# Optimization experiments

Measured on AMD Instinct MI355X. Metric: run time of the kernel, lower is better.

## Reference

```python
import jax, jax.numpy as jnp
import numpy as np

NEG_RATIO = 3.0
EPS = 1e-4
WEIGHT = 1.0
LOG_CLAMP = -100.0  # torch.nn.BCELoss clamps log terms at -100

B, H, W = 32, 768, 768


def setup_inputs() -> dict:
    key = jax.random.key(0)
    k1, k2 = jax.random.split(key)
    gt_centerness = jax.random.uniform(k1, (B, H, W), dtype=jnp.float32)
    pred_binary = jax.random.uniform(k2, (B, 1, H, W), dtype=jnp.float32)
    return {"gt_centerness": gt_centerness, "pred_binary": pred_binary}


def reference(gt_centerness, pred_binary):
    b = pred_binary.shape[0]
    # squeeze pred channel dim, flatten per-batch then logically treat as flat
    pred = pred_binary.reshape(b, -1)          # [B, N]
    gt = gt_centerness.reshape(b, -1)          # [B, N]
    dtype = pred.dtype

    pos_mask = gt >= 0.9                        # hard positives
    ignore_mask = (gt >= 0.8) & (gt < 0.9)      # ignore band
    mask = 1.0 - ignore_mask.astype(dtype)      # keep = 1, ignore = 0

    # elementwise BCE with torch-style log clamping
    loss = -(gt * jnp.clip(jnp.log(pred), LOG_CLAMP, None)
             + (1.0 - gt) * jnp.clip(jnp.log(1.0 - pred), LOG_CLAMP, None))

    pos = jnp.sum(pos_mask)                                  # scalar int
    ignore = jnp.sum(ignore_mask)
    total = gt.size
    neg = total - pos - ignore

    positive_sum = jnp.sum(loss * mask * pos_mask.astype(dtype))

    neg_mask = (1.0 - pos_mask.astype(dtype)) * mask
    neg_loss = (loss * neg_mask).reshape(-1)                 # [B*N]

    # k = min(max(pos,1) * neg_ratio, neg), as an integer
    k = jnp.minimum(jnp.maximum(pos, 1).astype(dtype) * NEG_RATIO,
                    neg.astype(dtype))
    k = jnp.floor(k).astype(jnp.int32)

    # top-k sum via descending sort + rank mask (k is traced -> fixed-shape)
    sorted_neg = jnp.sort(neg_loss)[::-1]
    ranks = jnp.arange(sorted_neg.shape[0], dtype=jnp.int32)
    topk_sum = jnp.sum(jnp.where(ranks < k, sorted_neg, jnp.zeros((), dtype)))

    denom = pos.astype(dtype) + k.astype(dtype) + EPS
    return WEIGHT * (NEG_RATIO * positive_sum + topk_sum) / denom
```

## Files before the change

kernel.cpp:

```cpp
#include <hip/hip_runtime.h>

#define NBINS    2048
#define REPL     4
#define THREADS  256
#define BLOCKS   512
#define CNTSH    44

__device__ __forceinline__ void process_elem(
    float g, float p,
    unsigned int& posc, float& ps,
    unsigned long long* hist, unsigned int repl)
{
    float nlp = fminf(-__logf(p), 100.0f);
    float nlq = fminf(-__logf(1.0f - p), 100.0f);
    float loss = fmaf(g, nlp - nlq, nlq);

    bool isPos = (g >= 0.9f);
    bool isNeg = (g < 0.8f);
    posc += isPos;
    if (isPos) ps += loss;
    if (isNeg) {
        unsigned int b = 0;
        if (loss > 0.0f) {
            b = __float_as_uint(loss) >> 20;
            if (b > NBINS - 1) b = NBINS - 1;
        }
        unsigned long long q =
            (unsigned long long)(unsigned int)(fmaf(loss, 1048576.0f, 0.5f));
        atomicAdd(&hist[(b << 2) | repl], (1ull << CNTSH) | q);
    }
}

__device__ __forceinline__ void process4(
    float4 g, float4 p,
    unsigned int& posc, float& ps,
    unsigned long long* hist, unsigned int repl)
{
    process_elem(g.x, p.x, posc, ps, hist, repl);
    process_elem(g.y, p.y, posc, ps, hist, repl);
    process_elem(g.z, p.z, posc, ps, hist, repl);
    process_elem(g.w, p.w, posc, ps, hist, repl);
}

__global__ __launch_bounds__(THREADS) void pass1(
    const float* __restrict__ gt, const float* __restrict__ pred,
    unsigned int* __restrict__ counts, unsigned long long* __restrict__ sums,
    unsigned int* __restrict__ posCnt, double* __restrict__ psum,
    int n4, int nTail, long long tailBase)
{
    __shared__ unsigned long long hist[NBINS * REPL];
    for (int i = threadIdx.x; i < NBINS * REPL; i += THREADS) hist[i] = 0ull;
    __syncthreads();

    unsigned int posc = 0;
    float ps = 0.0f;
    const unsigned int repl = threadIdx.x & (REPL - 1);

    const float4* g4p = (const float4*)gt;
    const float4* p4p = (const float4*)pred;
    const int stride = gridDim.x * blockDim.x;
    int i = blockIdx.x * blockDim.x + threadIdx.x;

    for (; i + 3 * stride < n4; i += 4 * stride) {
        float4 g0 = g4p[i];              float4 p0 = p4p[i];
        float4 g1 = g4p[i + stride];     float4 p1 = p4p[i + stride];
        float4 g2 = g4p[i + 2 * stride]; float4 p2 = p4p[i + 2 * stride];
        float4 g3 = g4p[i + 3 * stride]; float4 p3 = p4p[i + 3 * stride];

        process4(g0, p0, posc, ps, hist, repl);
        process4(g1, p1, posc, ps, hist, repl);
        process4(g2, p2, posc, ps, hist, repl);
        process4(g3, p3, posc, ps, hist, repl);
    }
    for (; i < n4; i += stride) {
        float4 g4 = g4p[i];
        float4 p4 = p4p[i];
        process4(g4, p4, posc, ps, hist, repl);
    }
    if (blockIdx.x == 0 && threadIdx.x < nTail) {
        long long e = tailBase + threadIdx.x;
        process_elem(gt[e], pred[e], posc, ps, hist, repl);
    }

    __syncthreads();
    for (int b = threadIdx.x; b < NBINS; b += THREADS) {
        unsigned long long v = hist[(b << 2) | 0] + hist[(b << 2) | 1]
                             + hist[(b << 2) | 2] + hist[(b << 2) | 3];
        if (v) {
            atomicAdd(&counts[b], (unsigned int)(v >> CNTSH));
            atomicAdd(&sums[b],   v & ((1ull << CNTSH) - 1));
        }
    }

    double pd = (double)ps;
    for (int off = 32; off > 0; off >>= 1) {
        posc += __shfl_down(posc, off);
        pd   += __shfl_down(pd, off);
    }
    if ((threadIdx.x & 63) == 0) {
        if (posc) atomicAdd(posCnt, posc);
        atomicAdd(psum, pd);
    }
}

__global__ __launch_bounds__(256) void finalize(
    const unsigned int* __restrict__ counts,
    const unsigned long long* __restrict__ sums,
    const unsigned int* __restrict__ posCnt, const double* __restrict__ psum,
    float* __restrict__ out)
{
    __shared__ unsigned long long scnt[256];
    __shared__ double             ssum[256];
    __shared__ int                s_chunk;
    __shared__ double             s_topk;

    const int t = threadIdx.x;
    const int BPT = NBINS / 256;
    const int base = t * BPT;
    const double INVFIX = 1.0 / 1048576.0;

    unsigned long long c = 0; double s = 0.0;
    #pragma unroll
    for (int i = 0; i < BPT; ++i) {
        c += counts[base + i];
        s += (double)sums[base + i] * INVFIX;
    }
    scnt[t] = c; ssum[t] = s;
    if (t == 0) { s_chunk = -1; s_topk = 0.0; }
    __syncthreads();

    for (int off = 1; off < 256; off <<= 1) {
        unsigned long long cv = (t + off < 256) ? scnt[t + off] : 0ull;
        double             sv = (t + off < 256) ? ssum[t + off] : 0.0;
        __syncthreads();
        scnt[t] += cv; ssum[t] += sv;
        __syncthreads();
    }

    const unsigned int pos = posCnt[0];
    const unsigned long long total = scnt[0];

    float kf = fminf(fmaxf((float)pos, 1.0f) * 3.0f, (float)total);
    long long k = (long long)floorf(kf);

    unsigned long long Sincl = scnt[t];
    unsigned long long Sexcl = (t < 255) ? scnt[t + 1] : 0ull;
    double SexclSum          = (t < 255) ? ssum[t + 1] : 0.0;

    if (k > 0 && Sexcl < (unsigned long long)k && Sincl >= (unsigned long long)k) {
        double topk = SexclSum;
        unsigned long long need = (unsigned long long)k - Sexcl;
        for (int i = BPT - 1; i >= 0 && need > 0; --i) {
            int b = base + i;
            unsigned long long cb = counts[b];
            if (!cb) continue;
            double sb = (double)sums[b] * INVFIX;
            if (cb <= need) {
                topk += sb;
                need -= cb;
            } else {
                float lo = __uint_as_float((unsigned)b << 20);
                float hi = (b + 1 < NBINS) ? __uint_as_float((unsigned)(b + 1) << 20) : lo;
                double w = (double)hi - (double)lo;
                double n = (double)cb;
                double r = (double)need;
                double mean = sb / n;
                topk += r * (mean + 0.5 * w * (1.0 - r / n));
                need = 0;
            }
        }
        s_topk = topk;
        s_chunk = t;
    }
    __syncthreads();

    if (t == 0) {
        double topk = (s_chunk >= 0) ? s_topk : 0.0;
        float denf = (float)pos + (float)k;
        denf += 1e-4f;
        double res = (3.0 * (*psum) + topk) / (double)denf;
        out[0] = (float)res;
    }
}

extern "C" void kernel_launch(void* const* d_in, const int* in_sizes, int n_in,
                              void* d_out, int out_size, void* d_ws, size_t ws_size,
                              hipStream_t stream) {
    const float* gt   = (const float*)d_in[0];
    const float* pred = (const float*)d_in[1];
    float* out = (float*)d_out;

    double*             psum   = (double*)d_ws;
    unsigned int*       posCnt = (unsigned int*)((char*)d_ws + 8);
    unsigned int*       counts = (unsigned int*)((char*)d_ws + 16);
    unsigned long long* sums   = (unsigned long long*)((char*)d_ws + 16 + NBINS * sizeof(unsigned int));

    size_t zbytes = 16 + (size_t)NBINS * (sizeof(unsigned int) + sizeof(unsigned long long));
    hipMemsetAsync(d_ws, 0, zbytes, stream);

    long long n = (long long)in_sizes[0];
    int n4 = (int)(n >> 2);
    int nTail = (int)(n & 3);
    long long tailBase = (long long)n4 * 4;

    pass1<<<dim3(BLOCKS), dim3(THREADS), 0, stream>>>(
        gt, pred, counts, sums, posCnt, psum, n4, nTail, tailBase);
    finalize<<<dim3(1), dim3(256), 0, stream>>>(counts, sums, posCnt, psum, out);
}
```

Before: 87.31 us.

## Double-buffer global loads with inline asm and explicit vmcnt waits in pass1

Adds a specialized path for the exact input size (36 strides per thread) that issues global_load_dwordx4 through inline asm into two register sets. It waits with s_waitcnt vmcnt(8) so one batch of eight loads stays in flight while the previous batch is processed. The aim is to keep memory requests outstanding during the log and histogram-atomic work instead of stalling on every batch. It raises register pressure, depends on hand-placed waitcnt correctness, and the generic fallback loop loses its 4x unroll.

New measurement: 91.91 us. +5.3%, slower.

```diff
diff --git a/kernel.cpp b/kernel.cpp
--- a/kernel.cpp
+++ b/kernel.cpp
@@ -5,6 +5,14 @@
 #define THREADS  256
 #define BLOCKS   512
 #define CNTSH    44
+#define STRIDE   (BLOCKS * THREADS)
+
+#define GLOAD(dst, ptr) \
+    asm volatile("global_load_dwordx4 %0, %1, off" : "=v"(dst) : "v"(ptr))
+#define VMWAIT8()  do { asm volatile("s_waitcnt vmcnt(8)" ::: "memory"); \
+                        __builtin_amdgcn_sched_barrier(0); } while (0)
+#define VMWAIT0()  do { asm volatile("s_waitcnt vmcnt(0)" ::: "memory"); \
+                        __builtin_amdgcn_sched_barrier(0); } while (0)
 
 __device__ __forceinline__ void process_elem(
     float g, float p,
@@ -42,6 +50,24 @@
     process_elem(g.w, p.w, posc, ps, hist, repl);
 }
 
+#define ISSUE(G0,P0,G1,P1,G2,P2,G3,P3, base) do {      \
+    GLOAD(G0, g4p + (base));                           \
+    GLOAD(P0, p4p + (base));                           \
+    GLOAD(G1, g4p + (base) + STRIDE);                  \
+    GLOAD(P1, p4p + (base) + STRIDE);                  \
+    GLOAD(G2, g4p + (base) + 2 * STRIDE);              \
+    GLOAD(P2, p4p + (base) + 2 * STRIDE);              \
+    GLOAD(G3, g4p + (base) + 3 * STRIDE);              \
+    GLOAD(P3, p4p + (base) + 3 * STRIDE);              \
+} while (0)
+
+#define PROC(G0,P0,G1,P1,G2,P2,G3,P3) do {             \
+    process4(G0, P0, posc, ps, hist, repl);            \
+    process4(G1, P1, posc, ps, hist, repl);            \
+    process4(G2, P2, posc, ps, hist, repl);            \
+    process4(G3, P3, posc, ps, hist, repl);            \
+} while (0)
+
 __global__ __launch_bounds__(THREADS) void pass1(
     const float* __restrict__ gt, const float* __restrict__ pred,
     unsigned int* __restrict__ counts, unsigned long long* __restrict__ sums,
@@ -58,24 +84,33 @@
 
     const float4* g4p = (const float4*)gt;
     const float4* p4p = (const float4*)pred;
-    const int stride = gridDim.x * blockDim.x;
-    int i = blockIdx.x * blockDim.x + threadIdx.x;
-
-    for (; i + 3 * stride < n4; i += 4 * stride) {
-        float4 g0 = g4p[i];              float4 p0 = p4p[i];
-        float4 g1 = g4p[i + stride];     float4 p1 = p4p[i + stride];
-        float4 g2 = g4p[i + 2 * stride]; float4 p2 = p4p[i + 2 * stride];
-        float4 g3 = g4p[i + 3 * stride]; float4 p3 = p4p[i + 3 * stride];
-
-        process4(g0, p0, posc, ps, hist, repl);
-        process4(g1, p1, posc, ps, hist, repl);
-        process4(g2, p2, posc, ps, hist, repl);
-        process4(g3, p3, posc, ps, hist, repl);
-    }
-    for (; i < n4; i += stride) {
-        float4 g4 = g4p[i];
-        float4 p4 = p4p[i];
-        process4(g4, p4, posc, ps, hist, repl);
+
+    if (n4 == 36 * STRIDE && gridDim.x == BLOCKS) {
+        const int i0 = blockIdx.x * THREADS + threadIdx.x;
+        float4 gA0,pA0,gA1,pA1,gA2,pA2,gA3,pA3;
+        float4 gB0,pB0,gB1,pB1,gB2,pB2,gB3,pB3;
+
+        ISSUE(gA0,pA0,gA1,pA1,gA2,pA2,gA3,pA3, i0);
+        int ip = i0;
+        #pragma unroll
+        for (int d = 0; d < 4; ++d) {
+            ISSUE(gB0,pB0,gB1,pB1,gB2,pB2,gB3,pB3, ip + 4 * STRIDE);
+            VMWAIT8();
+            PROC(gA0,pA0,gA1,pA1,gA2,pA2,gA3,pA3);
+            ISSUE(gA0,pA0,gA1,pA1,gA2,pA2,gA3,pA3, ip + 8 * STRIDE);
+            VMWAIT8();
+            PROC(gB0,pB0,gB1,pB1,gB2,pB2,gB3,pB3);
+            ip += 8 * STRIDE;
+        }
+        VMWAIT0();
+        PROC(gA0,pA0,gA1,pA1,gA2,pA2,gA3,pA3);
+    } else {
+        const int stride = gridDim.x * blockDim.x;
+        for (int i = blockIdx.x * blockDim.x + threadIdx.x; i < n4; i += stride) {
+            float4 g4 = g4p[i];
+            float4 p4 = p4p[i];
+            process4(g4, p4, posc, ps, hist, repl);
+        }
     }
     if (blockIdx.x == 0 && threadIdx.x < nTail) {
         long long e = tailBase + threadIdx.x;
```

## Software-pipeline global loads with inline asm and explicit vmcnt waits

Applied to the files above, without the earlier changes.

Replaces the strided main loop with a fully unrolled, five-stage software pipeline for the exact problem size (36 strides per thread). It issues raw global_load_dwordx4 via inline asm and uses s_waitcnt vmcnt plus sched barriers so up to 32 loads stay in flight while earlier batches are processed. The goal is to hide memory latency behind the log and atomic histogram work. It uses many VGPRs (40 float4 buffers), which may reduce occupancy or cause spills, and it falls back to a simple loop for other sizes.

Measured after the change: 99.90 us. 1.14x slower.

```diff
diff --git a/kernel.cpp b/kernel.cpp
--- a/kernel.cpp
+++ b/kernel.cpp
@@ -5,6 +5,13 @@
 #define THREADS  256
 #define BLOCKS   512
 #define CNTSH    44
+#define STRIDE   (BLOCKS * THREADS)
+#define BS       (4 * STRIDE)
+
+#define GLOAD(dst, ptr) \
+    asm volatile("global_load_dwordx4 %0, %1, off" : "=v"(dst) : "v"(ptr))
+#define VMWAIT(N) do { asm volatile("s_waitcnt vmcnt(" #N ")" ::: "memory"); \
+                       __builtin_amdgcn_sched_barrier(0); } while (0)
 
 __device__ __forceinline__ void process_elem(
     float g, float p,
@@ -42,6 +49,24 @@
     process_elem(g.w, p.w, posc, ps, hist, repl);
 }
 
+#define ISSUE(s, base) do {                                 \
+    GLOAD(g##s##0, g4p + (base));                           \
+    GLOAD(p##s##0, p4p + (base));                           \
+    GLOAD(g##s##1, g4p + (base) + STRIDE);                  \
+    GLOAD(p##s##1, p4p + (base) + STRIDE);                  \
+    GLOAD(g##s##2, g4p + (base) + 2 * STRIDE);              \
+    GLOAD(p##s##2, p4p + (base) + 2 * STRIDE);              \
+    GLOAD(g##s##3, g4p + (base) + 3 * STRIDE);              \
+    GLOAD(p##s##3, p4p + (base) + 3 * STRIDE);              \
+} while (0)
+
+#define PROCS(s) do {                                       \
+    process4(g##s##0, p##s##0, posc, ps, hist, repl);       \
+    process4(g##s##1, p##s##1, posc, ps, hist, repl);       \
+    process4(g##s##2, p##s##2, posc, ps, hist, repl);       \
+    process4(g##s##3, p##s##3, posc, ps, hist, repl);       \
+} while (0)
+
 __global__ __launch_bounds__(THREADS) void pass1(
     const float* __restrict__ gt, const float* __restrict__ pred,
     unsigned int* __restrict__ counts, unsigned long long* __restrict__ sums,
@@ -58,24 +83,37 @@
 
     const float4* g4p = (const float4*)gt;
     const float4* p4p = (const float4*)pred;
-    const int stride = gridDim.x * blockDim.x;
-    int i = blockIdx.x * blockDim.x + threadIdx.x;
-
-    for (; i + 3 * stride < n4; i += 4 * stride) {
-        float4 g0 = g4p[i];              float4 p0 = p4p[i];
-        float4 g1 = g4p[i + stride];     float4 p1 = p4p[i + stride];
-        float4 g2 = g4p[i + 2 * stride]; float4 p2 = p4p[i + 2 * stride];
-        float4 g3 = g4p[i + 3 * stride]; float4 p3 = p4p[i + 3 * stride];
-
-        process4(g0, p0, posc, ps, hist, repl);
-        process4(g1, p1, posc, ps, hist, repl);
-        process4(g2, p2, posc, ps, hist, repl);
-        process4(g3, p3, posc, ps, hist, repl);
-    }
-    for (; i < n4; i += stride) {
-        float4 g4 = g4p[i];
-        float4 p4 = p4p[i];
-        process4(g4, p4, posc, ps, hist, repl);
+
+    if (n4 == 36 * STRIDE && gridDim.x == BLOCKS) {
+        const int i0 = blockIdx.x * THREADS + threadIdx.x;
+        float4 gA0,gA1,gA2,gA3,pA0,pA1,pA2,pA3;
+        float4 gB0,gB1,gB2,gB3,pB0,pB1,pB2,pB3;
+        float4 gC0,gC1,gC2,gC3,pC0,pC1,pC2,pC3;
+        float4 gD0,gD1,gD2,gD3,pD0,pD1,pD2,pD3;
+        float4 gE0,gE1,gE2,gE3,pE0,pE1,pE2,pE3;
+
+        ISSUE(A, i0);
+        ISSUE(B, i0 + 1 * BS);
+        ISSUE(C, i0 + 2 * BS);
+        ISSUE(D, i0 + 3 * BS);
+
+        ISSUE(E, i0 + 4 * BS);  VMWAIT(32);  PROCS(A);
+        ISSUE(A, i0 + 5 * BS);  VMWAIT(32);  PROCS(B);
+        ISSUE(B, i0 + 6 * BS);  VMWAIT(32);  PROCS(C);
+        ISSUE(C, i0 + 7 * BS);  VMWAIT(32);  PROCS(D);
+        ISSUE(D, i0 + 8 * BS);  VMWAIT(32);  PROCS(E);
+
+        VMWAIT(24);  PROCS(A);
+        VMWAIT(16);  PROCS(B);
+        VMWAIT(8);   PROCS(C);
+        VMWAIT(0);   PROCS(D);
+    } else {
+        const int stride = gridDim.x * blockDim.x;
+        for (int i = blockIdx.x * blockDim.x + threadIdx.x; i < n4; i += stride) {
+            float4 g4 = g4p[i];
+            float4 p4 = p4p[i];
+            process4(g4, p4, posc, ps, hist, repl);
+        }
     }
     if (blockIdx.x == 0 && threadIdx.x < nTail) {
         long long e = tailBase + threadIdx.x;
```
